# Kernel tuning notes

Hardware: AMD Instinct MI355X
Metric: run time of the kernel (lower is better)

## Reference

```python
import jax, jax.numpy as jnp
import numpy as np
import math

D_MODEL = 2048
N_HEADS = 16
D_HEAD = D_MODEL // N_HEADS
D_FF = 8192
B = 2
S = 2048
LN_EPS = 1e-5


def _rope_tables(s, d_head):
    inv_freq = 1.0 / (10000.0 ** (np.arange(0, d_head, 2, dtype=np.float32) / d_head))
    t = np.arange(s, dtype=np.float32)
    freqs = np.outer(t, inv_freq)                      # [s, d_head/2]
    emb = np.concatenate([freqs, freqs], axis=-1)      # [s, d_head]
    cos = jnp.asarray(np.cos(emb))[None, None]         # [1,1,s,d_head]
    sin = jnp.asarray(np.sin(emb))[None, None]
    return cos, sin


def setup_inputs() -> dict:
    key = jax.random.key(0)
    ks = jax.random.split(key, 12)
    x = jax.random.normal(ks[0], (B, S, D_MODEL), dtype=jnp.float32)
    cos, sin = _rope_tables(S, D_HEAD)
    # additive causal mask
    mask = jnp.where(jnp.tril(jnp.ones((S, S), dtype=bool)), 0.0, -1e9).astype(jnp.float32)[None, None]
    s_in = 1.0 / math.sqrt(D_MODEL)
    s_ff = 1.0 / math.sqrt(D_FF)
    params = {
        "ln1_g": jnp.ones((D_MODEL,), jnp.float32),
        "ln1_b": jnp.zeros((D_MODEL,), jnp.float32),
        "w_qkv": jax.random.uniform(ks[1], (D_MODEL, 3 * D_MODEL), jnp.float32, -s_in, s_in),
        "b_qkv": jax.random.uniform(ks[2], (3 * D_MODEL,), jnp.float32, -s_in, s_in),
        "w_out": jax.random.uniform(ks[3], (D_MODEL, D_MODEL), jnp.float32, -s_in, s_in),
        "b_out": jax.random.uniform(ks[4], (D_MODEL,), jnp.float32, -s_in, s_in),
        "ln2_g": jnp.ones((D_MODEL,), jnp.float32),
        "ln2_b": jnp.zeros((D_MODEL,), jnp.float32),
        "w_ff1": jax.random.uniform(ks[5], (D_MODEL, D_FF), jnp.float32, -s_in, s_in),
        "b_ff1": jax.random.uniform(ks[6], (D_FF,), jnp.float32, -s_in, s_in),
        "w_ff2": jax.random.uniform(ks[7], (D_FF, D_MODEL), jnp.float32, -s_ff, s_ff),
        "b_ff2": jax.random.uniform(ks[8], (D_MODEL,), jnp.float32, -s_ff, s_ff),
    }
    return {"x": x, "cos": cos, "sin": sin, "mask": mask, **params}


def _layernorm(x, g, b):
    m = jnp.mean(x, axis=-1, keepdims=True)
    v = jnp.var(x, axis=-1, keepdims=True)
    return (x - m) * jax.lax.rsqrt(v + LN_EPS) * g + b


def _rotate_half(x):
    x1, x2 = jnp.split(x, 2, axis=-1)
    return jnp.concatenate([-x2, x1], axis=-1)


def reference(x, cos, sin, mask,
              ln1_g, ln1_b, w_qkv, b_qkv, w_out, b_out,
              ln2_g, ln2_b, w_ff1, b_ff1, w_ff2, b_ff2):
    b, s, d = x.shape
    # attention sub-block (dropout = identity, eval mode)
    xn = _layernorm(x, ln1_g, ln1_b)
    qkv = (xn @ w_qkv + b_qkv).reshape(b, s, 3, N_HEADS, D_HEAD)
    qkv = jnp.transpose(qkv, (2, 0, 3, 1, 4))           # [3,b,h,s,dh]
    q, k, v = qkv[0], qkv[1], qkv[2]
    q = q * cos + _rotate_half(q) * sin
    k = k * cos + _rotate_half(k) * sin
    scale = 1.0 / math.sqrt(D_HEAD)
    attn = jnp.einsum('bhqd,bhkd->bhqk', q, k) * scale + mask
    attn = jax.nn.softmax(attn, axis=-1)
    a_out = jnp.einsum('bhqk,bhkd->bhqd', attn, v)
    a_out = jnp.transpose(a_out, (0, 2, 1, 3)).reshape(b, s, d)
    x = x + (a_out @ w_out + b_out)
    # MLP sub-block (exact GELU, matching torch nn.GELU default)
    xn = _layernorm(x, ln2_g, ln2_b)
    h = jax.nn.gelu(xn @ w_ff1 + b_ff1, approximate=False)
    x = x + (h @ w_ff2 + b_ff2)
    return x
```

## Files before the change

### kernel.cpp

```cpp
#include <hip/hip_runtime.h>
#include <hip/hip_bf16.h>
#include <math.h>

typedef __hip_bfloat16 bf16;
using bf16x8 = __bf16 __attribute__((ext_vector_type(8)));
using f32x4  = float  __attribute__((ext_vector_type(4)));

#define D_MODEL 2048
#define S_LEN   2048
#define NB      2
#define NH      16
#define DHEAD   128
#define DFF     8192
#define M_ROWS  (NB * S_LEN)

__device__ __forceinline__ void gload_lds16(const void* g, void* l) {
    __builtin_amdgcn_global_load_lds((const __attribute__((address_space(1))) void*)g,
                                     (__attribute__((address_space(3))) void*)l, 16, 0, 0);
}

__global__ __launch_bounds__(256) void ln_kernel(const float* __restrict__ x,
                                                 const float* __restrict__ gw,
                                                 const float* __restrict__ bw,
                                                 bf16* __restrict__ out) {
    const int row = blockIdx.x;
    const float* xr = x + (size_t)row * D_MODEL;
    const int tid = threadIdx.x;
    float4 v0 = ((const float4*)xr)[tid * 2];
    float4 v1 = ((const float4*)xr)[tid * 2 + 1];
    float s = v0.x + v0.y + v0.z + v0.w + v1.x + v1.y + v1.z + v1.w;
    float q = v0.x*v0.x + v0.y*v0.y + v0.z*v0.z + v0.w*v0.w
            + v1.x*v1.x + v1.y*v1.y + v1.z*v1.z + v1.w*v1.w;
    #pragma unroll
    for (int off = 32; off; off >>= 1) {
        s += __shfl_xor(s, off);
        q += __shfl_xor(q, off);
    }
    __shared__ float red[8];
    const int wid = tid >> 6;
    if ((tid & 63) == 0) { red[wid] = s; red[4 + wid] = q; }
    __syncthreads();
    s = red[0] + red[1] + red[2] + red[3];
    q = red[4] + red[5] + red[6] + red[7];
    const float mean = s * (1.0f / D_MODEL);
    const float var  = q * (1.0f / D_MODEL) - mean * mean;
    const float inv  = rsqrtf(var + 1e-5f);
    float4 g0 = ((const float4*)gw)[tid * 2];
    float4 g1 = ((const float4*)gw)[tid * 2 + 1];
    float4 b0 = ((const float4*)bw)[tid * 2];
    float4 b1 = ((const float4*)bw)[tid * 2 + 1];
    bf16* orow = out + (size_t)row * D_MODEL + tid * 8;
    orow[0] = __float2bfloat16((v0.x - mean) * inv * g0.x + b0.x);
    orow[1] = __float2bfloat16((v0.y - mean) * inv * g0.y + b0.y);
    orow[2] = __float2bfloat16((v0.z - mean) * inv * g0.z + b0.z);
    orow[3] = __float2bfloat16((v0.w - mean) * inv * g0.w + b0.w);
    orow[4] = __float2bfloat16((v1.x - mean) * inv * g1.x + b1.x);
    orow[5] = __float2bfloat16((v1.y - mean) * inv * g1.y + b1.y);
    orow[6] = __float2bfloat16((v1.z - mean) * inv * g1.z + b1.z);
    orow[7] = __float2bfloat16((v1.w - mean) * inv * g1.w + b1.w);
}

__global__ __launch_bounds__(256) void transpose_f2b(const float* __restrict__ in,
                                                     bf16* __restrict__ out,
                                                     int R, int C) {
    __shared__ float t[32][33];
    const int c0 = blockIdx.x * 32, r0 = blockIdx.y * 32;
    const int tx = threadIdx.x & 31, ty = threadIdx.x >> 5;
    #pragma unroll
    for (int i = ty; i < 32; i += 8) t[i][tx] = in[(size_t)(r0 + i) * C + c0 + tx];
    __syncthreads();
    #pragma unroll
    for (int i = ty; i < 32; i += 8)
        out[(size_t)(c0 + i) * R + r0 + tx] = __float2bfloat16(t[tx][i]);
}

__global__ __launch_bounds__(256) void transpose_v(const bf16* __restrict__ in,
                                                   bf16* __restrict__ out) {
    const int bh = blockIdx.z;
    const bf16* ib = in + (size_t)bh * S_LEN * DHEAD;
    bf16* ob = out + (size_t)bh * DHEAD * S_LEN;
    __shared__ float t[32][33];
    const int c0 = blockIdx.x * 32;
    const int r0 = blockIdx.y * 32;
    const int tx = threadIdx.x & 31, ty = threadIdx.x >> 5;
    #pragma unroll
    for (int i = ty; i < 32; i += 8)
        t[i][tx] = __bfloat162float(ib[(size_t)(r0 + i) * DHEAD + c0 + tx]);
    __syncthreads();
    #pragma unroll
    for (int i = ty; i < 32; i += 8)
        ob[(size_t)(c0 + i) * S_LEN + r0 + tx] = __float2bfloat16(t[tx][i]);
}

__global__ __launch_bounds__(256) void rope_kernel(bf16* __restrict__ qk,
                                                   const float* __restrict__ ct,
                                                   const float* __restrict__ st) {
    const size_t idx = (size_t)blockIdx.x * 256 + threadIdx.x;
    const int dh = (int)(idx & 63);
    const size_t rrow = idx >> 6;
    const int sidx = (int)(rrow & (S_LEN - 1));
    const int which = (int)(rrow >> 16);
    const float f = (which == 0) ? 0.08838834764831845f : 1.0f;
    bf16* p = qk + rrow * DHEAD;
    const float c  = ct[sidx * DHEAD + dh];
    const float sn = st[sidx * DHEAD + dh];
    const float x1 = __bfloat162float(p[dh]);
    const float x2 = __bfloat162float(p[dh + 64]);
    p[dh]      = __float2bfloat16((x1 * c - x2 * sn) * f);
    p[dh + 64] = __float2bfloat16((x2 * c + x1 * sn) * f);
}

template <int EPI>
__global__ __launch_bounds__(256) void gemm_kernel(const bf16* __restrict__ A,
                                                   const bf16* __restrict__ Bt,
                                                   const float* __restrict__ bias,
                                                   const float* __restrict__ resid,
                                                   void* __restrict__ outp,
                                                   int M, int N, int K) {
    __shared__ __align__(16) bf16 As[128][64];
    __shared__ __align__(16) bf16 Bs[128][64];
    const int tid  = threadIdx.x;
    const int lane = tid & 63;
    const int wid  = tid >> 6;
    const int wr = wid >> 1, wc = wid & 1;
    const int cc = lane & 15, g = lane >> 4;
    const int csw = cc & 7;
    const int m0 = blockIdx.y * 128, n0 = blockIdx.x * 128;
    const int srow  = lane >> 3;
    const int sslot = (lane & 7) ^ (srow & 7);
    const int sb    = sslot * 16;

    f32x4 acc[4][4];
    const f32x4 zero = {0.f, 0.f, 0.f, 0.f};
    #pragma unroll
    for (int i = 0; i < 4; i++)
        #pragma unroll
        for (int j = 0; j < 4; j++) acc[i][j] = zero;

    const char* gA = (const char*)A  + ((size_t)(m0 + wid * 32 + srow) * K) * 2 + sb;
    const char* gB = (const char*)Bt + ((size_t)(n0 + wid * 32 + srow) * K) * 2 + sb;
    char* lA = (char*)&As[0][0] + wid * 4096;
    char* lB = (char*)&Bs[0][0] + wid * 4096;
    const size_t rowK2 = (size_t)K * 2;

    for (int k0 = 0; k0 < K; k0 += 64) {
        #pragma unroll
        for (int c = 0; c < 4; ++c) {
            gload_lds16(gA + (size_t)k0 * 2 + (size_t)c * 8 * rowK2, lA + c * 1024);
            gload_lds16(gB + (size_t)k0 * 2 + (size_t)c * 8 * rowK2, lB + c * 1024);
        }
        __syncthreads();
        #pragma unroll
        for (int kh = 0; kh < 2; kh++) {
            const int ux = ((kh * 4 + g) ^ csw) << 4;
            bf16x8 af[4], bfm[4];
            #pragma unroll
            for (int mi = 0; mi < 4; mi++)
                af[mi]  = *(const bf16x8*)((const char*)&As[wr * 64 + mi * 16 + cc][0] + ux);
            #pragma unroll
            for (int ni = 0; ni < 4; ni++)
                bfm[ni] = *(const bf16x8*)((const char*)&Bs[wc * 64 + ni * 16 + cc][0] + ux);
            #pragma unroll
            for (int mi = 0; mi < 4; mi++)
                #pragma unroll
                for (int ni = 0; ni < 4; ni++)
                    acc[mi][ni] = __builtin_amdgcn_mfma_f32_16x16x32_bf16(af[mi], bfm[ni], acc[mi][ni], 0, 0, 0);
        }
        __syncthreads();
    }

    #pragma unroll
    for (int mi = 0; mi < 4; mi++) {
        #pragma unroll
        for (int ni = 0; ni < 4; ni++) {
            const int colb = n0 + wc * 64 + ni * 16 + cc;
            const float bcol = bias[colb];
            #pragma unroll
            for (int r = 0; r < 4; r++) {
                const int row = m0 + wr * 64 + mi * 16 + g * 4 + r;
                const float v = acc[mi][ni][r] + bcol;
                if (EPI == 0) {
                    const int which = colb >> 11;
                    const int h     = (colb >> 7) & 15;
                    const int dh    = colb & 127;
                    const int b     = row >> 11;
                    const int sidx  = row & (S_LEN - 1);
                    bf16* o = (bf16*)outp;
                    o[((size_t)(which * 32 + b * 16 + h) * S_LEN + sidx) * DHEAD + dh] = __float2bfloat16(v);
                } else if (EPI == 1) {
                    float* o = (float*)outp;
                    o[(size_t)row * N + colb] = v + resid[(size_t)row * N + colb];
                } else {
                    bf16* o = (bf16*)outp;
                    const float gel = 0.5f * v * (1.0f + erff(v * 0.70710678118f));
                    o[(size_t)row * N + colb] = __float2bfloat16(gel);
                }
            }
        }
    }
}

__global__ __launch_bounds__(256) void attn_kernel(const bf16* __restrict__ q,
                                                   const bf16* __restrict__ k,
                                                   const bf16* __restrict__ vT,
                                                   bf16* __restrict__ aout) {
    const int qt = (int)(gridDim.x - 1 - blockIdx.x);
    const int bh = blockIdx.y;
    const int tid = threadIdx.x;
    const int lane = tid & 63, wid = tid >> 6;
    const int cc = lane & 15, g = lane >> 4;
    const int csw = cc & 7;
    const int q0 = qt * 64;
    const int q0w = q0 + wid * 16;
    const bf16* qb = q  + (size_t)bh * S_LEN * DHEAD;
    const char* kb2 = (const char*)(k  + (size_t)bh * S_LEN * DHEAD);
    const char* vb2 = (const char*)(vT + (size_t)bh * DHEAD * S_LEN);

    __shared__ __align__(16) bf16 Ks[2][64][128];
    __shared__ __align__(16) bf16 Vs[2][128][64];
    __shared__ __align__(16) bf16 Ps[4][16][72];

    const int kst_row = wid * 4 + (lane >> 4);
    const int kst_sl  = (lane & 15) ^ (kst_row & 7);
    const int vst_row = wid * 8 + (lane >> 3);
    const int vst_sl  = (lane & 7) ^ (vst_row & 7);

    bf16x8 qf[4];
    #pragma unroll
    for (int kk = 0; kk < 4; kk++)
        qf[kk] = *(const bf16x8*)(qb + (size_t)(q0w + cc) * DHEAD + kk * 32 + g * 8);

    f32x4 oacc[8];
    const f32x4 zero = {0.f, 0.f, 0.f, 0.f};
    #pragma unroll
    for (int d = 0; d < 8; d++) oacc[d] = zero;
    float lsum[4] = {0.f, 0.f, 0.f, 0.f};

    {
        char* ksl = (char*)&Ks[0][0][0] + wid * 1024;
        char* vsl = (char*)&Vs[0][0][0] + wid * 1024;
        #pragma unroll
        for (int i = 0; i < 4; ++i) {
            gload_lds16(kb2 + (size_t)(kst_row + i * 16) * 256 + kst_sl * 16, ksl + i * 4096);
            gload_lds16(vb2 + (size_t)(vst_row + i * 32) * (S_LEN * 2) + vst_sl * 16, vsl + i * 4096);
        }
    }
    asm volatile("s_waitcnt vmcnt(0)" ::: "memory");
    __syncthreads();

    int cur = 0;
    for (int kt = 0; kt <= qt; ++kt) {
        const int kv0 = kt * 64;
        if (kt < qt) {
            const int nv0 = kv0 + 64;
            char* ksl = (char*)&Ks[cur ^ 1][0][0] + wid * 1024;
            char* vsl = (char*)&Vs[cur ^ 1][0][0] + wid * 1024;
            #pragma unroll
            for (int i = 0; i < 4; ++i) {
                gload_lds16(kb2 + (size_t)(nv0 + kst_row + i * 16) * 256 + kst_sl * 16, ksl + i * 4096);
                gload_lds16(vb2 + (size_t)(vst_row + i * 32) * (S_LEN * 2) + (size_t)nv0 * 2 + vst_sl * 16, vsl + i * 4096);
            }
        }

        f32x4 sacc[4];
        #pragma unroll
        for (int ni = 0; ni < 4; ni++) sacc[ni] = zero;
        __builtin_amdgcn_s_setprio(1);
        #pragma unroll
        for (int kk = 0; kk < 4; kk++) {
            const int ux = ((kk * 4 + g) ^ csw) << 4;
            #pragma unroll
            for (int ni = 0; ni < 4; ni++) {
                const bf16x8 kf = *(const bf16x8*)((const char*)&Ks[cur][ni * 16 + cc][0] + ux);
                sacc[ni] = __builtin_amdgcn_mfma_f32_16x16x32_bf16(qf[kk], kf, sacc[ni], 0, 0, 0);
            }
        }
        __builtin_amdgcn_s_setprio(0);

        #pragma unroll
        for (int r = 0; r < 4; r++) {
            const int qrow = q0w + g * 4 + r;
            float p[4];
            #pragma unroll
            for (int ni = 0; ni < 4; ni++) {
                const float sv = (kv0 + ni * 16 + cc <= qrow) ? sacc[ni][r] : -1e30f;
                p[ni] = __expf(sv);
            }
            lsum[r] += (p[0] + p[1]) + (p[2] + p[3]);
            #pragma unroll
            for (int ni = 0; ni < 4; ni++)
                Ps[wid][g * 4 + r][ni * 16 + cc] = __float2bfloat16(p[ni]);
        }

        __builtin_amdgcn_s_setprio(1);
        #pragma unroll
        for (int ks = 0; ks < 2; ks++) {
            const bf16x8 pf = *(const bf16x8*)(&Ps[wid][cc][ks * 32 + g * 8]);
            const int ux = ((ks * 4 + g) ^ csw) << 4;
            #pragma unroll
            for (int d = 0; d < 8; d++) {
                const bf16x8 vf = *(const bf16x8*)((const char*)&Vs[cur][d * 16 + cc][0] + ux);
                oacc[d] = __builtin_amdgcn_mfma_f32_16x16x32_bf16(pf, vf, oacc[d], 0, 0, 0);
            }
        }
        __builtin_amdgcn_s_setprio(0);

        asm volatile("s_waitcnt vmcnt(0)" ::: "memory");
        __syncthreads();
        cur ^= 1;
    }

    const int b = bh >> 4, h = bh & 15;
    #pragma unroll
    for (int r = 0; r < 4; r++) {
        float rs = lsum[r];
        #pragma unroll
        for (int off = 1; off < 16; off <<= 1) rs += __shfl_xor(rs, off);
        const float invl = 1.0f / rs;
        const int srow = q0w + g * 4 + r;
        bf16* orow = aout + ((size_t)(b * S_LEN + srow)) * D_MODEL + h * DHEAD;
        #pragma unroll
        for (int d = 0; d < 8; d++) orow[d * 16 + cc] = __float2bfloat16(oacc[d][r] * invl);
    }
}

extern "C" void kernel_launch(void* const* d_in, const int* in_sizes, int n_in,
                              void* d_out, int out_size, void* d_ws, size_t ws_size,
                              hipStream_t stream) {
    (void)in_sizes; (void)n_in; (void)out_size; (void)ws_size;
    const float* x      = (const float*)d_in[0];
    const float* cosb   = (const float*)d_in[1];
    const float* sinb   = (const float*)d_in[2];
    const float* ln1_g  = (const float*)d_in[4];
    const float* ln1_b  = (const float*)d_in[5];
    const float* w_qkv  = (const float*)d_in[6];
    const float* b_qkv  = (const float*)d_in[7];
    const float* w_out  = (const float*)d_in[8];
    const float* b_out  = (const float*)d_in[9];
    const float* ln2_g  = (const float*)d_in[10];
    const float* ln2_b  = (const float*)d_in[11];
    const float* w_ff1  = (const float*)d_in[12];
    const float* b_ff1  = (const float*)d_in[13];
    const float* w_ff2  = (const float*)d_in[14];
    const float* b_ff2  = (const float*)d_in[15];
    float* out = (float*)d_out;

    char* ws = (char*)d_ws;
    bf16* wT_qkv = (bf16*)(ws + 0);
    bf16* wT_out = (bf16*)(ws + 25165824);
    bf16* wT_ff1 = (bf16*)(ws + 33554432);
    bf16* wT_ff2 = (bf16*)(ws + 67108864);
    bf16* xn     = (bf16*)(ws + 100663296);
    bf16* qkv    = (bf16*)(ws + 117440512);
    bf16* aoutb  = (bf16*)(ws + 167772160);
    bf16* vTb    = (bf16*)(ws + 184549376);
    bf16* hbuf   = (bf16*)(ws + 117440512);
    bf16* kbuf = qkv + (size_t)32 * S_LEN * DHEAD;
    bf16* vbuf = qkv + (size_t)64 * S_LEN * DHEAD;

    transpose_f2b<<<dim3(192, 64),  256, 0, stream>>>(w_qkv, wT_qkv, 2048, 6144);
    transpose_f2b<<<dim3(64, 64),   256, 0, stream>>>(w_out, wT_out, 2048, 2048);
    transpose_f2b<<<dim3(256, 64),  256, 0, stream>>>(w_ff1, wT_ff1, 2048, 8192);
    transpose_f2b<<<dim3(64, 256),  256, 0, stream>>>(w_ff2, wT_ff2, 8192, 2048);

    ln_kernel<<<M_ROWS, 256, 0, stream>>>(x, ln1_g, ln1_b, xn);
    gemm_kernel<0><<<dim3(48, 32), 256, 0, stream>>>(xn, wT_qkv, b_qkv, nullptr, qkv, M_ROWS, 6144, 2048);
    rope_kernel<<<32768, 256, 0, stream>>>(qkv, cosb, sinb);
    transpose_v<<<dim3(4, 64, 32), 256, 0, stream>>>(vbuf, vTb);
    attn_kernel<<<dim3(32, 32), 256, 0, stream>>>(qkv, kbuf, vTb, aoutb);
    gemm_kernel<1><<<dim3(16, 32), 256, 0, stream>>>(aoutb, wT_out, b_out, x, out, M_ROWS, 2048, 2048);
    ln_kernel<<<M_ROWS, 256, 0, stream>>>(out, ln2_g, ln2_b, xn);
    gemm_kernel<2><<<dim3(64, 32), 256, 0, stream>>>(xn, wT_ff1, b_ff1, nullptr, hbuf, M_ROWS, DFF, 2048);
    gemm_kernel<1><<<dim3(16, 32), 256, 0, stream>>>(hbuf, wT_ff2, b_ff2, out, out, M_ROWS, 2048, DFF);
}
```

Measured before the change: 773.5 us.

## Split-K the FF2 GEMM and remap workgroups across XCDs

The FF2 GEMM (K=8192, only 512 tiles) is split into two K halves launched as a 3D grid. Each half writes fp32 partials into the workspace, and a new combine kernel adds both partials, the bias and the residual. All GEMM and attention kernels also remap flat block IDs so that consecutive IDs are spread across the 8 XCDs, which is meant to improve L2 locality. The trade is more parallelism and better cache reuse for FF2 against an extra 64MB partial write and read plus one more kernel launch.

```diff
diff --git a/kernel.cpp b/kernel.cpp
--- a/kernel.cpp
+++ b/kernel.cpp
@@ -116,7 +116,7 @@
                                                    const float* __restrict__ bias,
                                                    const float* __restrict__ resid,
                                                    void* __restrict__ outp,
-                                                   int M, int N, int K) {
+                                                   int M, int N, int K, int kLen) {
     __shared__ __align__(16) bf16 As[128][64];
     __shared__ __align__(16) bf16 Bs[128][64];
     const int tid  = threadIdx.x;
@@ -125,7 +125,18 @@
     const int wr = wid >> 1, wc = wid & 1;
     const int cc = lane & 15, g = lane >> 4;
     const int csw = cc & 7;
-    const int m0 = blockIdx.y * 128, n0 = blockIdx.x * 128;
+
+    const int nx = gridDim.x, ny = gridDim.y, nz = gridDim.z;
+    int flat = blockIdx.x + nx * (blockIdx.y + ny * blockIdx.z);
+    const int nwg = nx * ny * nz;
+    flat = (flat & 7) * (nwg >> 3) + (flat >> 3);
+    const int bx = flat % nx;
+    const int t2 = flat / nx;
+    const int by = t2 % ny;
+    const int bz = t2 / ny;
+    const int m0 = by * 128, n0 = bx * 128;
+    const int kStart = bz * kLen;
+
     const int srow  = lane >> 3;
     const int sslot = (lane & 7) ^ (srow & 7);
     const int sb    = sslot * 16;
@@ -143,7 +154,7 @@
     char* lB = (char*)&Bs[0][0] + wid * 4096;
     const size_t rowK2 = (size_t)K * 2;
 
-    for (int k0 = 0; k0 < K; k0 += 64) {
+    for (int k0 = kStart; k0 < kStart + kLen; k0 += 64) {
         #pragma unroll
         for (int c = 0; c < 4; ++c) {
             gload_lds16(gA + (size_t)k0 * 2 + (size_t)c * 8 * rowK2, lA + c * 1024);
@@ -174,7 +185,7 @@
         #pragma unroll
         for (int ni = 0; ni < 4; ni++) {
             const int colb = n0 + wc * 64 + ni * 16 + cc;
-            const float bcol = bias[colb];
+            const float bcol = (EPI == 3) ? 0.0f : bias[colb];
             #pragma unroll
             for (int r = 0; r < 4; r++) {
                 const int row = m0 + wr * 64 + mi * 16 + g * 4 + r;
@@ -190,22 +201,44 @@
                 } else if (EPI == 1) {
                     float* o = (float*)outp;
                     o[(size_t)row * N + colb] = v + resid[(size_t)row * N + colb];
-                } else {
+                } else if (EPI == 2) {
                     bf16* o = (bf16*)outp;
                     const float gel = 0.5f * v * (1.0f + erff(v * 0.70710678118f));
                     o[(size_t)row * N + colb] = __float2bfloat16(gel);
+                } else {
+                    float* o = (float*)outp + (size_t)bz * M * N;
+                    o[(size_t)row * N + colb] = v;
                 }
             }
         }
     }
+}
+
+__global__ __launch_bounds__(256) void ff2_combine(const float* __restrict__ p,
+                                                   const float* __restrict__ bias,
+                                                   float* __restrict__ out) {
+    const size_t i4 = (size_t)blockIdx.x * 256 + threadIdx.x;
+    const float4 a  = ((const float4*)out)[i4];
+    const float4 p0 = ((const float4*)p)[i4];
+    const float4 p1 = ((const float4*)(p + (size_t)M_ROWS * D_MODEL))[i4];
+    const float4 b  = ((const float4*)bias)[i4 & (D_MODEL / 4 - 1)];
+    float4 r;
+    r.x = a.x + p0.x + p1.x + b.x;
+    r.y = a.y + p0.y + p1.y + b.y;
+    r.z = a.z + p0.z + p1.z + b.z;
+    r.w = a.w + p0.w + p1.w + b.w;
+    ((float4*)out)[i4] = r;
 }
 
 __global__ __launch_bounds__(256) void attn_kernel(const bf16* __restrict__ q,
                                                    const bf16* __restrict__ k,
                                                    const bf16* __restrict__ vT,
                                                    bf16* __restrict__ aout) {
-    const int qt = (int)(gridDim.x - 1 - blockIdx.x);
-    const int bh = blockIdx.y;
+    int flat = blockIdx.x + gridDim.x * blockIdx.y;
+    const int nwg = gridDim.x * gridDim.y;
+    flat = (flat & 7) * (nwg >> 3) + (flat >> 3);
+    const int qt = (int)(gridDim.x - 1 - (flat % gridDim.x));
+    const int bh = flat / gridDim.x;
     const int tid = threadIdx.x;
     const int lane = tid & 63, wid = tid >> 6;
     const int cc = lane & 15, g = lane >> 4;
@@ -355,6 +388,7 @@
     bf16* aoutb  = (bf16*)(ws + 167772160);
     bf16* vTb    = (bf16*)(ws + 184549376);
     bf16* hbuf   = (bf16*)(ws + 117440512);
+    float* partial = (float*)(ws + 0);
     bf16* kbuf = qkv + (size_t)32 * S_LEN * DHEAD;
     bf16* vbuf = qkv + (size_t)64 * S_LEN * DHEAD;
 
@@ -364,12 +398,13 @@
     transpose_f2b<<<dim3(64, 256),  256, 0, stream>>>(w_ff2, wT_ff2, 8192, 2048);
 
     ln_kernel<<<M_ROWS, 256, 0, stream>>>(x, ln1_g, ln1_b, xn);
-    gemm_kernel<0><<<dim3(48, 32), 256, 0, stream>>>(xn, wT_qkv, b_qkv, nullptr, qkv, M_ROWS, 6144, 2048);
+    gemm_kernel<0><<<dim3(48, 32), 256, 0, stream>>>(xn, wT_qkv, b_qkv, nullptr, qkv, M_ROWS, 6144, 2048, 2048);
     rope_kernel<<<32768, 256, 0, stream>>>(qkv, cosb, sinb);
     transpose_v<<<dim3(4, 64, 32), 256, 0, stream>>>(vbuf, vTb);
     attn_kernel<<<dim3(32, 32), 256, 0, stream>>>(qkv, kbuf, vTb, aoutb);
-    gemm_kernel<1><<<dim3(16, 32), 256, 0, stream>>>(aoutb, wT_out, b_out, x, out, M_ROWS, 2048, 2048);
+    gemm_kernel<1><<<dim3(16, 32), 256, 0, stream>>>(aoutb, wT_out, b_out, x, out, M_ROWS, 2048, 2048, 2048);
     ln_kernel<<<M_ROWS, 256, 0, stream>>>(out, ln2_g, ln2_b, xn);
-    gemm_kernel<2><<<dim3(64, 32), 256, 0, stream>>>(xn, wT_ff1, b_ff1, nullptr, hbuf, M_ROWS, DFF, 2048);
-    gemm_kernel<1><<<dim3(16, 32), 256, 0, stream>>>(hbuf, wT_ff2, b_ff2, out, out, M_ROWS, 2048, DFF);
-}
+    gemm_kernel<2><<<dim3(64, 32), 256, 0, stream>>>(xn, wT_ff1, b_ff1, nullptr, hbuf, M_ROWS, DFF, 2048, 2048);
+    gemm_kernel<3><<<dim3(16, 32, 2), 256, 0, stream>>>(hbuf, wT_ff2, nullptr, nullptr, partial, M_ROWS, 2048, 8192, 4096);
+    ff2_combine<<<8192, 256, 0, stream>>>(partial, b_ff2, out);
+}
```

Measured after the change: 799.4 us. 3.3% more time.
